# Kernel optimization log

Hardware: AMD Instinct MI355X
Metric: run time of the kernel (lower is better)

## Reference

```python
import jax, jax.numpy as jnp
import numpy as np

N, IN, OUT, T = 262144, 128, 128, 8

def setup_inputs() -> dict:
    key = jax.random.key(0)
    k1, k2, k3, k4 = jax.random.split(key, 4)
    x = jax.random.normal(k1, (N, IN), dtype=jnp.float32)
    x_type = jax.random.randint(k2, (N,), 0, T, dtype=jnp.int32)
    bound = 1.0 / np.sqrt(IN)
    # TypedLinear weight: [num_types, in_size, out_size]
    W = jax.random.uniform(k3, (T, IN, OUT), minval=-bound, maxval=bound, dtype=jnp.float32)
    b = jax.random.uniform(k4, (T, OUT), minval=-bound, maxval=bound, dtype=jnp.float32)
    return {"x": x, "x_type": x_type, "W": W, "b": b}

def reference(x, x_type, W, b):
    # Per-sample typed linear: out[n] = x[n] @ W[x_type[n]] + b[x_type[n]]
    # Grouped-GEMM formulation: loop over the small fixed set of types,
    # masking contributions, to avoid gathering a [N, IN, OUT] weight tensor.
    num_types = W.shape[0]
    out = jnp.zeros((x.shape[0], W.shape[2]), dtype=x.dtype)
    for t in range(num_types):
        mask = (x_type == t).astype(x.dtype)[:, None]  # [N,1]
        out = out + (x @ W[t]) * mask
    out = out + b[x_type]  # type-indexed bias gather
    return out
```

## Files before the change

kernel.cpp:

```cpp
#include <hip/hip_runtime.h>
#include <hip/hip_bf16.h>

#define N_ROWS 262144
#define IN_DIM 128
#define OUT_DIM 128
#define NTYPES 8
#define ROWS_PER_BLOCK 256
#define GROUP_M 16
#define MAX_GROUPS 32
#define ROW_PAD 132

typedef short bf16x8 __attribute__((ext_vector_type(8)));
typedef float f32x4 __attribute__((ext_vector_type(4)));

__device__ __forceinline__ unsigned short f2bf_rne(float f) {
    unsigned int u = __float_as_uint(f);
    u += 0x7fff + ((u >> 16) & 1);
    return (unsigned short)(u >> 16);
}

__global__ void __launch_bounds__(128) prep_w_kernel(const float* __restrict__ W,
                                                     unsigned short* __restrict__ Wb) {
    const int t = blockIdx.x >> 7;
    const int o = blockIdx.x & 127;
    const int i = threadIdx.x;
    Wb[(t * OUT_DIM + o) * IN_DIM + i] = f2bf_rne(W[(t * IN_DIM + i) * OUT_DIM + o]);
}

__device__ __forceinline__ bf16x8 cvt_8f32_to_bf16(f32x4 f0, f32x4 f1) {
    union { bf16x8 v; __hip_bfloat162 h[4]; } u;
    u.h[0] = __float22bfloat162_rn(make_float2(f0[0], f0[1]));
    u.h[1] = __float22bfloat162_rn(make_float2(f0[2], f0[3]));
    u.h[2] = __float22bfloat162_rn(make_float2(f1[0], f1[1]));
    u.h[3] = __float22bfloat162_rn(make_float2(f1[2], f1[3]));
    return u.v;
}

__global__ void __launch_bounds__(256, 4) typed_linear_kernel(
        const float* __restrict__ x, const int* __restrict__ xt,
        const unsigned short* __restrict__ Wb, const float* __restrict__ bias,
        float* __restrict__ out) {
    __shared__ float s_out[4][GROUP_M * ROW_PAD];
    __shared__ int s_cnt[NTYPES];
    __shared__ int s_cursor[NTYPES];
    __shared__ unsigned short s_list[ROWS_PER_BLOCK];
    __shared__ unsigned char s_gtype[MAX_GROUPS];
    __shared__ short s_gstart[MAX_GROUPS];
    __shared__ unsigned char s_gcnt[MAX_GROUPS];
    __shared__ int s_ngroups;
    __shared__ float s_bias[NTYPES * OUT_DIM];

    const int tid = threadIdx.x;
    const int row0 = blockIdx.x * ROWS_PER_BLOCK;

    if (tid < NTYPES) s_cnt[tid] = 0;
    __syncthreads();
    const int my_t = xt[row0 + tid];
    atomicAdd(&s_cnt[my_t], 1);
    reinterpret_cast<float4*>(s_bias)[tid] = reinterpret_cast<const float4*>(bias)[tid];
    __syncthreads();
    if (tid == 0) {
        int acc = 0, g = 0;
        for (int i = 0; i < NTYPES; ++i) {
            int c = s_cnt[i];
            s_cursor[i] = acc;
            for (int s = 0; s < c; s += GROUP_M) {
                s_gtype[g] = (unsigned char)i;
                s_gstart[g] = (short)(acc + s);
                s_gcnt[g] = (unsigned char)((c - s) < GROUP_M ? (c - s) : GROUP_M);
                ++g;
            }
            acc += c;
        }
        s_ngroups = g;
    }
    __syncthreads();
    {
        int pos = atomicAdd(&s_cursor[my_t], 1);
        s_list[pos] = (unsigned short)tid;
    }
    __syncthreads();

    const int wave = tid >> 6;
    const int lane = tid & 63;
    const int m = lane & 15;
    const int q = lane >> 4;
    const int ngroups = s_ngroups;
    float* sow = s_out[wave];

    for (int g = wave; g < ngroups; g += 4) {
        const int t  = s_gtype[g];
        const int gs = s_gstart[g];
        const int gc = s_gcnt[g];

        const int mm0 = (m < gc) ? m : (gc - 1);
        const float* ap0 = x + (size_t)(row0 + s_list[gs + mm0]) * IN_DIM + q * 8;
        bf16x8 afrag[4];
        #pragma unroll
        for (int kc = 0; kc < 4; ++kc) {
            const f32x4 f0 = *reinterpret_cast<const f32x4*>(ap0 + kc * 32);
            const f32x4 f1 = *reinterpret_cast<const f32x4*>(ap0 + kc * 32 + 4);
            afrag[kc] = cvt_8f32_to_bf16(f0, f1);
        }

        const unsigned short* wt = Wb + t * (IN_DIM * OUT_DIM);
        const float* sb = s_bias + t * OUT_DIM;

        f32x4 acc[8];
        #pragma unroll
        for (int nt = 0; nt < 8; ++nt) {
            const unsigned short* wcol = wt + (nt * 16 + m) * IN_DIM + q * 8;
            bf16x8 bfr[4];
            #pragma unroll
            for (int kc = 0; kc < 4; ++kc)
                bfr[kc] = *reinterpret_cast<const bf16x8*>(wcol + kc * 32);
            f32x4 a = {0.f, 0.f, 0.f, 0.f};
            #pragma unroll
            for (int kc = 0; kc < 4; ++kc)
                a = __builtin_amdgcn_mfma_f32_16x16x32_bf16(afrag[kc], bfr[kc], a, 0, 0, 0);
            acc[nt] = a;
        }

        #pragma unroll
        for (int nt = 0; nt < 8; ++nt) {
            const float bv = sb[nt * 16 + m];
            #pragma unroll
            for (int r = 0; r < 4; ++r)
                sow[(q * 4 + r) * ROW_PAD + nt * 16 + m] = acc[nt][r] + bv;
        }

        const int half = lane >> 5;
        const int c4 = (lane & 31) * 4;
        #pragma unroll
        for (int j = 0; j < 8; ++j) {
            const int rr = j * 2 + half;
            if (rr < gc) {
                const int orow = row0 + s_list[gs + rr];
                const f32x4 v = *reinterpret_cast<const f32x4*>(&sow[rr * ROW_PAD + c4]);
                *reinterpret_cast<f32x4*>(&out[(size_t)orow * OUT_DIM + c4]) = v;
            }
        }
    }
}

extern "C" void kernel_launch(void* const* d_in, const int* in_sizes, int n_in,
                              void* d_out, int out_size, void* d_ws, size_t ws_size,
                              hipStream_t stream) {
    const float* x  = (const float*)d_in[0];
    const int* xt   = (const int*)d_in[1];
    const float* W  = (const float*)d_in[2];
    const float* b  = (const float*)d_in[3];
    float* out      = (float*)d_out;
    unsigned short* Wb = (unsigned short*)d_ws;

    prep_w_kernel<<<NTYPES * OUT_DIM, 128, 0, stream>>>(W, Wb);
    typed_linear_kernel<<<N_ROWS / ROWS_PER_BLOCK, 256, 0, stream>>>(x, xt, Wb, b, out);
}
```

Measured before the change: 315.6 us.

## Halve rows per block, shrink LDS epilogue, move bias to registers for occupancy

Cuts rows per block from 256 to 128 and raises the launch-bounds minimum to 8 blocks per SM. LDS use drops: the per-wave output staging buffer is halved by writing the 16x128 tile in two 64-column passes, and the shared bias table is removed, with bias read from global into registers. The aim is more resident waves to hide the memory latency of x loads and output stores. In exchange, smaller blocks produce more partially filled 16-row groups, which wastes MFMA work and repeats reads of the type's weights.

```diff
diff --git a/kernel.cpp b/kernel.cpp
--- a/kernel.cpp
+++ b/kernel.cpp
@@ -5,10 +5,10 @@
 #define IN_DIM 128
 #define OUT_DIM 128
 #define NTYPES 8
-#define ROWS_PER_BLOCK 256
+#define ROWS_PER_BLOCK 128
 #define GROUP_M 16
-#define MAX_GROUPS 32
-#define ROW_PAD 132
+#define MAX_GROUPS 16
+#define EPI_COLS 68
 
 typedef short bf16x8 __attribute__((ext_vector_type(8)));
 typedef float f32x4 __attribute__((ext_vector_type(4)));
@@ -36,11 +36,11 @@
     return u.v;
 }
 
-__global__ void __launch_bounds__(256, 4) typed_linear_kernel(
+__global__ void __launch_bounds__(256, 8) typed_linear_kernel(
         const float* __restrict__ x, const int* __restrict__ xt,
         const unsigned short* __restrict__ Wb, const float* __restrict__ bias,
         float* __restrict__ out) {
-    __shared__ float s_out[4][GROUP_M * ROW_PAD];
+    __shared__ float s_out[4][GROUP_M * EPI_COLS];
     __shared__ int s_cnt[NTYPES];
     __shared__ int s_cursor[NTYPES];
     __shared__ unsigned short s_list[ROWS_PER_BLOCK];
@@ -48,16 +48,17 @@
     __shared__ short s_gstart[MAX_GROUPS];
     __shared__ unsigned char s_gcnt[MAX_GROUPS];
     __shared__ int s_ngroups;
-    __shared__ float s_bias[NTYPES * OUT_DIM];
 
     const int tid = threadIdx.x;
     const int row0 = blockIdx.x * ROWS_PER_BLOCK;
 
     if (tid < NTYPES) s_cnt[tid] = 0;
     __syncthreads();
-    const int my_t = xt[row0 + tid];
-    atomicAdd(&s_cnt[my_t], 1);
-    reinterpret_cast<float4*>(s_bias)[tid] = reinterpret_cast<const float4*>(bias)[tid];
+    int my_t = -1;
+    if (tid < ROWS_PER_BLOCK) {
+        my_t = xt[row0 + tid];
+        atomicAdd(&s_cnt[my_t], 1);
+    }
     __syncthreads();
     if (tid == 0) {
         int acc = 0, g = 0;
@@ -75,7 +76,7 @@
         s_ngroups = g;
     }
     __syncthreads();
-    {
+    if (tid < ROWS_PER_BLOCK) {
         int pos = atomicAdd(&s_cursor[my_t], 1);
         s_list[pos] = (unsigned short)tid;
     }
@@ -104,7 +105,10 @@
         }
 
         const unsigned short* wt = Wb + t * (IN_DIM * OUT_DIM);
-        const float* sb = s_bias + t * OUT_DIM;
+        float bv[8];
+        #pragma unroll
+        for (int nt = 0; nt < 8; ++nt)
+            bv[nt] = bias[t * OUT_DIM + nt * 16 + m];
 
         f32x4 acc[8];
         #pragma unroll
@@ -122,22 +126,24 @@
         }
 
         #pragma unroll
-        for (int nt = 0; nt < 8; ++nt) {
-            const float bv = sb[nt * 16 + m];
+        for (int pass = 0; pass < 2; ++pass) {
             #pragma unroll
-            for (int r = 0; r < 4; ++r)
-                sow[(q * 4 + r) * ROW_PAD + nt * 16 + m] = acc[nt][r] + bv;
-        }
-
-        const int half = lane >> 5;
-        const int c4 = (lane & 31) * 4;
-        #pragma unroll
-        for (int j = 0; j < 8; ++j) {
-            const int rr = j * 2 + half;
-            if (rr < gc) {
-                const int orow = row0 + s_list[gs + rr];
-                const f32x4 v = *reinterpret_cast<const f32x4*>(&sow[rr * ROW_PAD + c4]);
-                *reinterpret_cast<f32x4*>(&out[(size_t)orow * OUT_DIM + c4]) = v;
+            for (int j = 0; j < 4; ++j) {
+                const int nt = pass * 4 + j;
+                #pragma unroll
+                for (int r = 0; r < 4; ++r)
+                    sow[(q * 4 + r) * EPI_COLS + j * 16 + m] = acc[nt][r] + bv[nt];
+            }
+            const int rsub = lane >> 4;
+            const int c4 = (lane & 15) * 4;
+            #pragma unroll
+            for (int j2 = 0; j2 < 4; ++j2) {
+                const int rr = j2 * 4 + rsub;
+                if (rr < gc) {
+                    const int orow = row0 + s_list[gs + rr];
+                    const f32x4 v = *reinterpret_cast<const f32x4*>(&sow[rr * EPI_COLS + c4]);
+                    *reinterpret_cast<f32x4*>(&out[(size_t)orow * OUT_DIM + pass * 64 + c4]) = v;
+                }
             }
         }
     }
```

Measured after the change: 351.4 us. 1.11x slower.
